# Optimization experiments

Hardware: AMD Instinct MI355X
Metric: run time of the kernel (lower is better)

The kernel has to match this reference:

```python
import jax, jax.numpy as jnp
import numpy as np
from jax.scipy.linalg import block_diag

NI, NO, NU, NH, NB = 32, 2, 10, 1024, 16384   # num_input, num_output, num_u, num_hidden, batch
N = NU // NO                                   # MPC horizon N = 5
M_INEQ = NU + NI * (N - 1)                     # 138 inequality constraints
EPS = 1e-4                                     # Q = L L^T + eps I
BN_EPS = 1e-5                                  # torch BatchNorm1d default eps
IPM_ITERS = 30                                 # fixed primal-dual interior-point iterations
NEG_SLOPE = 0.2
SIGMA = 0.1                                    # centering parameter


def setup_inputs():
    key = jax.random.key(0)
    k = jax.random.split(key, 12)
    u = lambda kk, shape, lim: jax.random.uniform(kk, shape, jnp.float32, -lim, lim)
    return {
        "x": jax.random.normal(k[0], (NB, NI), jnp.float32),
        "fc1_w": u(k[1], (NH, NI), 1.0 / np.sqrt(NI)),
        "fc1_b": u(k[2], (NH,), 1.0 / np.sqrt(NI)),
        "fc2_w": u(k[3], (NU, NH), 1.0 / np.sqrt(NH)),
        "fc2_b": u(k[4], (NU,), 1.0 / np.sqrt(NH)),
        "bn1_g": jnp.ones((NH,), jnp.float32),
        "bn1_b": jnp.zeros((NH,), jnp.float32),
        "bn2_g": jnp.ones((NU,), jnp.float32),
        "bn2_b": jnp.zeros((NU,), jnp.float32),
        "L": jnp.tril(jax.random.uniform(k[5], (NI, NI), dtype=jnp.float32)),
        "L_P": jnp.tril(jax.random.uniform(k[6], (NI, NI), dtype=jnp.float32)),
        "L_R": jnp.tril(jax.random.uniform(k[7], (NO, NO), dtype=jnp.float32)),
        "A": u(k[8], (NI, NI), 1.0) * 0.1,   # scaled for stable A^k powers in B_hat
        "Bm": u(k[9], (NI, NO), 1.0),
        "u0": jnp.zeros((NU,), jnp.float32),
        "s0": jnp.ones((M_INEQ,), jnp.float32),
    }


def _bn(x, g, b):
    # training-mode BatchNorm1d: biased batch statistics
    mu = jnp.mean(x, axis=0)
    var = jnp.mean(jnp.square(x - mu), axis=0)
    return (x - mu) * jax.lax.rsqrt(var + BN_EPS) * g + b


def _build_qp(L, L_P, L_R, A, Bm, u0, s0):
    # Q = (tril mask * L)(...)^T + eps I, same for P (state) and R (input) costs
    Lm = jnp.tril(L);   Q = Lm @ Lm.T + EPS * jnp.eye(NI, dtype=L.dtype)
    Lp = jnp.tril(L_P); P = Lp @ Lp.T + EPS * jnp.eye(NI, dtype=L.dtype)
    Lr = jnp.tril(L_R); R = Lr @ Lr.T + EPS * jnp.eye(NO, dtype=L.dtype)
    # B_hat: lower block-Toeplitz with block (i,j) = A^{i-j} B for j<=i  -> [NI*(N-1), NU]
    pows = [Bm]
    for _ in range(N - 2):
        pows.append(A @ pows[-1])
    zero = jnp.zeros((NI, NO), dtype=L.dtype)
    rows = []
    for i in range(N - 1):
        blocks = [pows[i - j] for j in range(i + 1)] + [zero] * (N - 1 - i)
        rows.append(jnp.concatenate(blocks, axis=1))
    B_hat = jnp.concatenate(rows, axis=0)
    Q_diag = block_diag(*([Q] * (N - 2) + [P]))        # diag(Q,...,Q,P)
    R_diag = block_diag(*([R] * N))                    # diag(R,...,R)
    Q_hat = B_hat.T @ Q_diag @ B_hat + R_diag          # [NU, NU]
    G = jnp.concatenate([jnp.eye(NU, dtype=L.dtype), B_hat], axis=0)  # [M_INEQ, NU]
    h = G @ u0 + s0
    return Q_hat, G, h


def _ipm_qp(Qm, p, G, h):
    """Batched primal-dual interior point: min_z 1/2 z^T Qm z + p^T z  s.t.  G z <= h.
    Qm [nz,nz], G [m,nz], h [m] shared; p [B,nz] batched. Returns z* [B,nz]."""
    B, nz = p.shape
    m = G.shape[0]

    def step(carry, _):
        z, s, lam = carry
        rd = z @ Qm + p + lam @ G                 # dual residual (Qm symmetric)
        rp = z @ G.T + s - h                      # primal residual
        mu = jnp.mean(s * lam, axis=-1, keepdims=True)
        rc = s * lam - SIGMA * mu                 # centered complementarity
        w = lam / s                               # [B, m]
        H = Qm + jnp.einsum('mi,bm,mj->bij', G, w, G)   # [B, nz, nz]
        rhs = -(rd + ((lam * rp - rc) / s) @ G)         # [B, nz]
        dz = jnp.linalg.solve(H, rhs[..., None])[..., 0]
        ds = -rp - dz @ G.T
        dlam = (-rc - lam * ds) / s
        # fraction-to-boundary step keeping s, lam > 0
        rs = jnp.where(ds < 0, -s / jnp.where(ds < 0, ds, -1.0), jnp.inf)
        rl = jnp.where(dlam < 0, -lam / jnp.where(dlam < 0, dlam, -1.0), jnp.inf)
        alpha = jnp.minimum(1.0, 0.99 * jnp.minimum(jnp.min(rs, -1), jnp.min(rl, -1)))[:, None]
        return (z + alpha * dz, s + alpha * ds, lam + alpha * dlam), None

    z0 = jnp.zeros_like(p)
    s_init = jnp.ones((B, m), p.dtype)
    l_init = jnp.ones((B, m), p.dtype)
    (z, _, _), _ = jax.lax.scan(step, (z0, s_init, l_init), None, length=IPM_ITERS)
    return z


def reference(x, fc1_w, fc1_b, fc2_w, fc2_b, bn1_g, bn1_b, bn2_g, bn2_b,
              L, L_P, L_R, A, Bm, u0, s0):
    h1 = jax.nn.leaky_relu(x @ fc1_w.T + fc1_b, NEG_SLOPE)
    h1 = _bn(h1, bn1_g, bn1_b)
    p = jax.nn.leaky_relu(h1 @ fc2_w.T + fc2_b, NEG_SLOPE)
    p = _bn(p, bn2_g, bn2_b)                       # [B, NU] = linear cost of QP
    Q_hat, G, hvec = _build_qp(L, L_P, L_R, A, Bm, u0, s0)
    z = _ipm_qp(Q_hat, p, G, hvec)                 # [B, NU]
    return z[:, 0]                                 # z @ e0 (weight = [1,0,...,0])


if __name__ == '__main__':
    out = reference(**setup_inputs())
    print(out.shape, out[:4])
```

## Files before the change

### kernel.cpp

```cpp
#include <hip/hip_runtime.h>
#include <math.h>

#define NIx 32
#define NOx 2
#define NUx 10
#define NHx 1024
#define NBx 16384
#define MIx 138
#define EPSQ 1e-4f
#define BNEPS 1e-5f
#define ITERS 30
#define SLOPE 0.2f
#define SIGMA_C 0.1f

#define QM_OFF 0
#define G_OFF 128
#define H_OFF 1856
#define P2_OFF 2048
#define P1S_OFF 2368
#define P1Q_OFF 6464
#define PRAW_OFF 10560

__device__ __forceinline__ float frcp(float x){ return __builtin_amdgcn_rcpf(x); }
__device__ __forceinline__ float frsq(float x){ return __builtin_amdgcn_rsqf(x); }
__device__ __forceinline__ float lrelu(float x){ return x > 0.0f ? x : SLOPE * x; }

typedef float v2f __attribute__((ext_vector_type(2)));
__device__ __forceinline__ v2f make2(float a, float b){ v2f r; r.x = a; r.y = b; return r; }
__device__ __forceinline__ v2f splat2(float a){ v2f r; r.x = a; r.y = a; return r; }
__device__ __forceinline__ v2f pkfma(v2f a, v2f b, v2f c){ return __builtin_elementwise_fma(a, b, c); }
__device__ __forceinline__ v2f pkmax(v2f a, v2f b){ return __builtin_elementwise_max(a, b); }

template<int CTRL>
__device__ __forceinline__ float dpp_mov(float x){
    int y = __builtin_amdgcn_update_dpp(0, __float_as_int(x), CTRL, 0xF, 0xF, true);
    return __int_as_float(y);
}
__device__ __forceinline__ float red8_add(float x){
    x += dpp_mov<0xB1>(x);
    x += dpp_mov<0x4E>(x);
    x += dpp_mov<0x141>(x);
    return x;
}
__device__ __forceinline__ float red8_max(float x){
    x = fmaxf(x, dpp_mov<0xB1>(x));
    x = fmaxf(x, dpp_mov<0x4E>(x));
    x = fmaxf(x, dpp_mov<0x141>(x));
    return x;
}

__global__ __launch_bounds__(256) void k_buildstats(const float* L, const float* LP, const float* LR,
                                                    const float* A, const float* Bm,
                                                    const float* u0, const float* s0,
                                                    const float* x, const float* w1, const float* b1,
                                                    float* ws){
    __shared__ float sL[1024], sLP[1024], sA[1024], sQ[1024], sP[1024];
    __shared__ float sPow[4][64];
    __shared__ float sBh[128*10];
    __shared__ float sQB[128*10];
    __shared__ float sR[3];
    __shared__ __align__(16) float sX[1024];
    int t = threadIdx.x;
    if (blockIdx.x < 2048){
        int rb = blockIdx.x >> 2;
        int cb = blockIdx.x & 3;
        int c = cb * 256 + t;
        const float4* wg4 = (const float4*)(w1 + (size_t)c * 32);
        float4 wr[8];
        #pragma unroll
        for (int q = 0; q < 8; ++q) wr[q] = wg4[q];
        float bc = b1[c];
        int r0 = rb * 32;
        const float4* xg4 = (const float4*)x + (size_t)r0 * 8;
        float4* sX4 = (float4*)sX;
        sX4[t] = xg4[t];
        __syncthreads();
        float sum = 0.0f, sq = 0.0f;
        #pragma unroll 2
        for (int r = 0; r < 32; ++r){
            const float4* xr4 = sX4 + r * 8;
            float a0 = 0, a1 = 0, a2 = 0, a3 = 0;
            #pragma unroll
            for (int q = 0; q < 8; ++q){
                float4 v = xr4[q];
                a0 = fmaf(v.x, wr[q].x, a0);
                a1 = fmaf(v.y, wr[q].y, a1);
                a2 = fmaf(v.z, wr[q].z, a2);
                a3 = fmaf(v.w, wr[q].w, a3);
            }
            float h = lrelu((a0 + a1) + (a2 + a3) + bc);
            sum += h; sq = fmaf(h, h, sq);
        }
        int buf = (rb & 3) * 1024 + c;
        atomicAdd(&ws[P1S_OFF + buf], sum);
        atomicAdd(&ws[P1Q_OFF + buf], sq);
        return;
    }
    for (int idx = t; idx < 1024; idx += 256){
        int i = idx >> 5, j = idx & 31;
        sL[idx]  = (j <= i) ? L[idx]  : 0.0f;
        sLP[idx] = (j <= i) ? LP[idx] : 0.0f;
        sA[idx]  = A[idx];
    }
    if (t < 64) sPow[0][t] = Bm[t];
    if (t == 0){
        float a = LR[0], b = LR[2], c = LR[3];
        sR[0] = a*a + EPSQ; sR[1] = a*b; sR[2] = b*b + c*c + EPSQ;
    }
    __syncthreads();
    for (int idx = t; idx < 1024; idx += 256){
        int i = idx >> 5, j = idx & 31;
        float q = 0.0f, p = 0.0f;
        for (int k = 0; k < 32; ++k){
            q = fmaf(sL[i*32+k],  sL[j*32+k],  q);
            p = fmaf(sLP[i*32+k], sLP[j*32+k], p);
        }
        if (i == j){ q += EPSQ; p += EPSQ; }
        sQ[idx] = q; sP[idx] = p;
    }
    for (int kp = 1; kp < 4; ++kp){
        __syncthreads();
        if (t < 64){
            int i = t >> 1, c = t & 1;
            float a = 0.0f;
            for (int j = 0; j < 32; ++j) a = fmaf(sA[i*32+j], sPow[kp-1][j*2+c], a);
            sPow[kp][t] = a;
        }
    }
    __syncthreads();
    for (int idx = t; idx < 1280; idx += 256){
        int r = idx / 10, c = idx % 10;
        int bi = r >> 5, ri = r & 31, bj = c >> 1, cj = c & 1;
        sBh[idx] = (bj <= bi) ? sPow[bi-bj][ri*2+cj] : 0.0f;
    }
    __syncthreads();
    for (int idx = t; idx < 1280; idx += 256){
        int r = idx / 10, c = idx % 10;
        int bi = r >> 5, ri = r & 31;
        const float* Qd = (bi < 3) ? sQ : sP;
        float a = 0.0f;
        for (int k = 0; k < 32; ++k) a = fmaf(Qd[ri*32+k], sBh[(bi*32+k)*10+c], a);
        sQB[idx] = a;
    }
    __syncthreads();
    if (t < 120){
        int i = t / 12, j = t % 12;
        float a = 0.0f;
        if (j < 10){
            for (int r = 0; r < 128; ++r) a = fmaf(sBh[r*10+i], sQB[r*10+j], a);
            if ((i >> 1) == (j >> 1)) a += sR[(i&1)+(j&1)];
        }
        ws[QM_OFF + t] = a;
    }
    for (int idx = t; idx < 144*12; idx += 256){
        int m = idx / 12, i = idx % 12;
        float v = 0.0f;
        if (i < 10 && m < MIx) v = (m < 10) ? ((i == m) ? 1.0f : 0.0f) : sBh[(m-10)*10 + i];
        ws[G_OFF + idx] = v;
    }
    for (int m = t; m < 144; m += 256){
        float hv = 0.0f;
        if (m < MIx){
            hv = s0[m];
            if (m < 10) hv += u0[m];
            else { for (int i = 0; i < 10; ++i) hv = fmaf(sBh[(m-10)*10+i], u0[i], hv); }
        }
        ws[H_OFF + m] = hv;
    }
}

__global__ __launch_bounds__(1024) void k_fc2(const float* __restrict__ x, const float* __restrict__ w1,
                                              const float* __restrict__ w2, const float* __restrict__ b1v,
                                              const float* __restrict__ b2v, const float* __restrict__ g1,
                                              const float* __restrict__ bb1, float* __restrict__ ws){
    __shared__ __align__(16) float sPool[10240];
    __shared__ float sA1[1024], sC1[1024];
    int t = threadIdx.x;
    if (t < 1024){
        int k = t;
        float ssum = 0.0f, qsum = 0.0f;
        #pragma unroll
        for (int b = 0; b < 4; ++b){
            ssum += ws[P1S_OFF + b*1024 + k];
            qsum += ws[P1Q_OFF + b*1024 + k];
        }
        float mu  = ssum * (1.0f/16384.0f);
        float var = qsum * (1.0f/16384.0f) - mu*mu;
        float a1 = g1[k] / sqrtf(var + BNEPS);
        sA1[k] = a1;
        sC1[k] = bb1[k] - mu * a1;
    }
    int r = t & 63;
    int q = t >> 6;
    int row = blockIdx.x * 64 + r;
    const float4* xg4 = (const float4*)(x + (size_t)row * 32);
    float4 xr[8];
    #pragma unroll
    for (int i = 0; i < 8; ++i) xr[i] = xg4[i];
    float acc[10];
    #pragma unroll
    for (int j = 0; j < 10; ++j) acc[j] = 0.0f;
    const float4* w1g4 = (const float4*)w1;
    float4* sW4 = (float4*)sPool;
    for (int ch = 0; ch < 8; ++ch){
        __syncthreads();
        if (t < 1024) sW4[t] = w1g4[ch*1024 + t];
        __syncthreads();
        #pragma unroll
        for (int i = 0; i < 8; ++i){
            int klc = __builtin_amdgcn_readfirstlane(q*8 + i);
            int kl  = __builtin_amdgcn_readfirstlane(ch*128 + klc);
            const float4* wv4 = sW4 + klc*8;
            float a0 = 0, a1 = 0, a2 = 0, a3 = 0;
            #pragma unroll
            for (int u = 0; u < 8; ++u){
                float4 wv = wv4[u];
                float4 xv = xr[u];
                a0 = fmaf(xv.x, wv.x, a0);
                a1 = fmaf(xv.y, wv.y, a1);
                a2 = fmaf(xv.z, wv.z, a2);
                a3 = fmaf(xv.w, wv.w, a3);
            }
            float h = fmaf(lrelu((a0 + a1) + (a2 + a3) + b1v[kl]), sA1[kl], sC1[kl]);
            #pragma unroll
            for (int j = 0; j < 10; ++j) acc[j] = fmaf(h, w2[j*1024 + kl], acc[j]);
        }
    }
    __syncthreads();
    float* pacc = sPool;
    #pragma unroll
    for (int j = 0; j < 10; ++j) pacc[t*10 + j] = acc[j];
    __syncthreads();
    if (t < 64){
        float pv[10];
        #pragma unroll
        for (int j = 0; j < 10; ++j){
            float a = b2v[j];
            #pragma unroll
            for (int w = 0; w < 16; ++w) a += pacc[(w*64 + t)*10 + j];
            pv[j] = lrelu(a);
        }
        #pragma unroll
        for (int j = 0; j < 10; ++j) ws[PRAW_OFF + (size_t)(blockIdx.x*64 + t)*10 + j] = pv[j];
        float sv[10], qv[10];
        #pragma unroll
        for (int j = 0; j < 10; ++j){ sv[j] = pv[j]; qv[j] = pv[j]*pv[j]; }
        #pragma unroll
        for (int m = 1; m < 64; m <<= 1){
            #pragma unroll
            for (int j = 0; j < 10; ++j){
                sv[j] += __shfl_xor(sv[j], m);
                qv[j] += __shfl_xor(qv[j], m);
            }
        }
        if (t == 0){
            int base = P2_OFF + (blockIdx.x & 15) * 20;
            #pragma unroll
            for (int j = 0; j < 10; ++j){
                atomicAdd(&ws[base + j], sv[j]);
                atomicAdd(&ws[base + 10 + j], qv[j]);
            }
        }
    }
}

#define TIX(i,j) ((i)*((i)+1)/2 + (j))

#define PSTEPA(P, B, GP) { \
    v2f sv = s2[P], lv = lam2[P]; \
    v2f isv; isv.x = frcp(sv.x); isv.y = frcp(sv.y); \
    v2f wv = lv * isv; \
    v2f r = sv - *(const v2f*)(sHH2 + (P)*16 + lg*2); \
    _Pragma("unroll") \
    for (int _i = 0; _i < (B); ++_i) r = pkfma(splat2(z[_i]), GP[_i], r); \
    rp2[P] = r; \
    sl2 = pkfma(sv, lv, sl2); \
    _Pragma("unroll") \
    for (int _i = 0; _i < (B); ++_i){ \
        v2f wg = wv * GP[_i]; \
        _Pragma("unroll") \
        for (int _j = 0; _j <= _i; ++_j) Hm2[TIX(_i,_j)] = pkfma(wg, GP[_j], Hm2[TIX(_i,_j)]); \
    } }

#define PSTEPB(P, B, GP) { \
    v2f sv = s2[P], lv = lam2[P]; \
    v2f isv; isv.x = frcp(sv.x); isv.y = frcp(sv.y); \
    v2f coef = pkfma(lv, rp2[P], smu2) * isv; \
    _Pragma("unroll") \
    for (int _i = 0; _i < (B); ++_i) racc2[_i] = pkfma(coef, GP[_i], racc2[_i]); }

#define PSTEPC(P, B, GP) { \
    v2f dotv = splat2(0.0f); \
    _Pragma("unroll") \
    for (int _i = 0; _i < (B); ++_i) dotv = pkfma(splat2(dz[_i]), GP[_i], dotv); \
    v2f sv = s2[P], lv = lam2[P]; \
    v2f isv; isv.x = frcp(sv.x); isv.y = frcp(sv.y); \
    v2f dsv = -(rp2[P] + dotv); \
    v2f rcv = pkfma(sv, lv, nsmu2); \
    v2f dlv = -(pkfma(lv, dsv, rcv) * isv); \
    ds2[P] = dsv; dl2[P] = dlv; \
    v2f ilv; ilv.x = frcp(lv.x); ilv.y = frcp(lv.y); \
    av2 = pkmax(av2, pkmax((-dsv)*isv, (-dlv)*ilv)); }

#define LOADP(GP, PP) v2f GP[8]; { \
    const float4* _g4 = (const float4*)(sG3 + lg*36 + (PP)*16); \
    float4 _a = _g4[0], _b = _g4[1], _c = _g4[2], _d = _g4[3]; \
    GP[0] = make2(_a.x,_a.y); GP[1] = make2(_a.z,_a.w); \
    GP[2] = make2(_b.x,_b.y); GP[3] = make2(_b.z,_b.w); \
    GP[4] = make2(_c.x,_c.y); GP[5] = make2(_c.z,_c.w); \
    GP[6] = make2(_d.x,_d.y); GP[7] = make2(_d.z,_d.w); }

__global__ __launch_bounds__(64, 2) void k_ipm(const float* __restrict__ ws, const float* __restrict__ g2v,
                                               const float* __restrict__ bb2, float* __restrict__ out){
    __shared__ __align__(16) float sQm[120];
    __shared__ __align__(16) float sQt2[72];
    __shared__ __align__(16) float sPV[8*12];
    __shared__ __align__(16) float sG3[8*36];
    __shared__ __align__(16) float sHH2[128];
    __shared__ float sA2[10], sC2[10];
    int t = threadIdx.x;
    for (int i = t; i < 120; i += 64) sQm[i] = ws[QM_OFF + i];
    if (t < 36){
        int i = 0;
        #pragma unroll
        for (int r = 1; r < 8; ++r) if (TIX(r,0) <= t) i = r;
        int j = t - TIX(i,0);
        sQt2[t*2]   = ws[QM_OFF + i*12 + j] * 0.125f;
        sQt2[t*2+1] = 0.0f;
    }
    if (t < 10){
        float ssum = 0.0f, qsum = 0.0f;
        #pragma unroll
        for (int b = 0; b < 16; ++b){
            ssum += ws[P2_OFF + b*20 + t];
            qsum += ws[P2_OFF + b*20 + 10 + t];
        }
        float mu  = ssum * (1.0f/16384.0f);
        float var = qsum * (1.0f/16384.0f) - mu*mu;
        float a2 = g2v[t] / sqrtf(var + BNEPS);
        sA2[t] = a2;
        sC2[t] = bb2[t] - mu * a2;
    }
    __syncthreads();

    int lg = t & 7;
    int eidx = t >> 3;
    int elem = blockIdx.x * 8 + eidx;
    const float* GB = ws + G_OFF;
    const float4* sQm4 = (const float4*)sQm;

    for (int i = t; i < 80; i += 64){
        int e = i / 10, c = i - e*10;
        int el = blockIdx.x * 8 + e;
        sPV[e*12 + c] = fmaf(ws[PRAW_OFF + (size_t)el*10 + c], sA2[c], sC2[c]);
    }
    for (int i = t; i < 128; i += 64){
        int c = i & 1, lgx = (i >> 1) & 7, p = i >> 4;
        int row = 10 + (p >> 1)*32 + (2*(p & 1) + c)*8 + lgx;
        sHH2[p*16 + lgx*2 + c] = ws[H_OFF + row];
    }
    for (int i = t; i < 256; i += 64){
        int c = i & 1, ii = (i >> 1) & 7, pp = (i >> 4) & 1, lgx = i >> 5;
        int row = 106 + (pp*2 + c)*8 + lgx;
        sG3[lgx*36 + pp*16 + ii*2 + c] = GB[row*12 + ii];
    }
    v2f g0[2], g1[2], g2r[4], g3r[4], g4r[6], g5r[6];
    {
        int ra, rb;
        ra = 10 + lg; rb = 18 + lg;
        #pragma unroll
        for (int i = 0; i < 2; ++i) g0[i] = make2(GB[ra*12+i], GB[rb*12+i]);
        ra = 26 + lg; rb = 34 + lg;
        #pragma unroll
        for (int i = 0; i < 2; ++i) g1[i] = make2(GB[ra*12+i], GB[rb*12+i]);
        ra = 42 + lg; rb = 50 + lg;
        #pragma unroll
        for (int i = 0; i < 4; ++i) g2r[i] = make2(GB[ra*12+i], GB[rb*12+i]);
        ra = 58 + lg; rb = 66 + lg;
        #pragma unroll
        for (int i = 0; i < 4; ++i) g3r[i] = make2(GB[ra*12+i], GB[rb*12+i]);
        ra = 74 + lg; rb = 82 + lg;
        #pragma unroll
        for (int i = 0; i < 6; ++i) g4r[i] = make2(GB[ra*12+i], GB[rb*12+i]);
        ra = 90 + lg; rb = 98 + lg;
        #pragma unroll
        for (int i = 0; i < 6; ++i) g5r[i] = make2(GB[ra*12+i], GB[rb*12+i]);
    }
    float h16 = ws[H_OFF + lg];
    float h17 = (lg < 2) ? ws[H_OFF + 8 + lg] : 1.0f;
    __syncthreads();

    float z[10];
    #pragma unroll
    for (int i = 0; i < 10; ++i) z[i] = 0.0f;
    v2f s2[8], lam2[8];
    #pragma unroll
    for (int p = 0; p < 8; ++p){ s2[p] = splat2(1.0f); lam2[p] = splat2(1.0f); }
    float s16v = 1.0f, s17v = 1.0f, lam16v = 1.0f;
    float lam17v = (lg < 2) ? 1.0f : 0.0f;

    #pragma unroll 1
    for (int it = 0; it < ITERS; ++it){
        v2f Hm2[36];
        {
            const v2f* qt2 = (const v2f*)sQt2;
            #pragma unroll
            for (int i = 0; i < 36; ++i) Hm2[i] = qt2[i];
        }
        v2f sl2 = splat2(0.0f);
        v2f rp2[8];
        float rp16, rp17;
        PSTEPA(0, 2, g0)  PSTEPA(1, 2, g1)
        PSTEPA(2, 4, g2r) PSTEPA(3, 4, g3r)
        PSTEPA(4, 6, g4r) PSTEPA(5, 6, g5r)
        { LOADP(gv, 0) PSTEPA(6, 8, gv) }
        { LOADP(gv, 1) PSTEPA(7, 8, gv) }
        float w16, w17, sl_s;
        {
            float zs = z[0];
            #pragma unroll
            for (int i = 1; i < 8; ++i) zs = (lg == i) ? z[i] : zs;
            rp16 = zs + s16v - h16;
            sl_s = s16v * lam16v;
            w16 = lam16v * frcp(s16v);
            float zs17 = (lg == 1) ? z[9] : z[8];
            rp17 = zs17 + s17v - h17;
            sl_s = fmaf(s17v, lam17v, sl_s);
            w17 = lam17v * frcp(s17v);
        }
        float Hm[55];
        #pragma unroll
        for (int i = 0; i < 36; ++i) Hm[i] = Hm2[i].x + Hm2[i].y;
        #pragma unroll
        for (int i = 0; i < 8; ++i) Hm[TIX(i,i)] += (lg == i) ? w16 : 0.0f;
        float d88 = (lg == 0) ? w17 : 0.0f;
        float d99 = (lg == 1) ? w17 : 0.0f;
        float sl = sl2.x + sl2.y + sl_s;
        #pragma unroll
        for (int i = 0; i < 36; ++i) Hm[i] = red8_add(Hm[i]);
        d88 = red8_add(d88);
        d99 = red8_add(d99);
        sl = red8_add(sl);
        float smu = SIGMA_C * sl * (1.0f/138.0f);
        __asm__ __volatile__("" ::: "memory");
        v2f smu2 = splat2(smu);
        v2f racc2[8];
        #pragma unroll
        for (int i = 0; i < 8; ++i) racc2[i] = splat2(0.0f);
        PSTEPB(0, 2, g0)  PSTEPB(1, 2, g1)
        PSTEPB(2, 4, g2r) PSTEPB(3, 4, g3r)
        PSTEPB(4, 6, g4r) PSTEPB(5, 6, g5r)
        { LOADP(gv, 0) PSTEPB(6, 8, gv) }
        { LOADP(gv, 1) PSTEPB(7, 8, gv) }
        float coef16 = frcp(s16v) * fmaf(lam16v, rp16, smu);
        float coef17 = frcp(s17v) * fmaf(lam17v, rp17, smu);
        coef17 = (lg < 2) ? coef17 : 0.0f;
        float rs[10];
        #pragma unroll
        for (int i = 0; i < 8; ++i){
            float v = racc2[i].x + racc2[i].y;
            v += (lg == i) ? coef16 : 0.0f;
            rs[i] = red8_add(v);
        }
        rs[8] = red8_add((lg == 0) ? coef17 : 0.0f);
        rs[9] = red8_add((lg == 1) ? coef17 : 0.0f);
        v2f rhs2[5];
        {
            const float4* pv4 = (const float4*)(sPV + eidx*12);
            float4 pa = pv4[0], pb = pv4[1];
            const float2* pv2 = (const float2*)(sPV + eidx*12 + 8);
            float2 pc = pv2[0];
            rhs2[0] = make2(-(pa.x + rs[0]), -(pa.y + rs[1]));
            rhs2[1] = make2(-(pa.z + rs[2]), -(pa.w + rs[3]));
            rhs2[2] = make2(-(pb.x + rs[4]), -(pb.y + rs[5]));
            rhs2[3] = make2(-(pb.z + rs[6]), -(pb.w + rs[7]));
            rhs2[4] = make2(-(pc.x + rs[8]), -(pc.y + rs[9]));
        }
        #pragma unroll
        for (int j = 0; j < 10; ++j){
            float4 qa = sQm4[j*3+0], qb = sQm4[j*3+1], qc = sQm4[j*3+2];
            v2f mz = splat2(-z[j]);
            rhs2[0] = pkfma(mz, make2(qa.x, qa.y), rhs2[0]);
            rhs2[1] = pkfma(mz, make2(qa.z, qa.w), rhs2[1]);
            rhs2[2] = pkfma(mz, make2(qb.x, qb.y), rhs2[2]);
            rhs2[3] = pkfma(mz, make2(qb.z, qb.w), rhs2[3]);
            rhs2[4] = pkfma(mz, make2(qc.x, qc.y), rhs2[4]);
            if (j >= 8){
                float q[10] = {qa.x,qa.y,qa.z,qa.w, qb.x,qb.y,qb.z,qb.w, qc.x,qc.y};
                #pragma unroll
                for (int i = 0; i <= j; ++i) Hm[TIX(j,i)] = q[i];
            }
        }
        Hm[TIX(8,8)] += d88;
        Hm[TIX(9,9)] += d99;
        float rhs[10] = {rhs2[0].x, rhs2[0].y, rhs2[1].x, rhs2[1].y, rhs2[2].x,
                         rhs2[2].y, rhs2[3].x, rhs2[3].y, rhs2[4].x, rhs2[4].y};
        #pragma unroll
        for (int j = 0; j < 10; ++j){
            float d = Hm[TIX(j,j)];
            #pragma unroll
            for (int k2 = 0; k2 < j; ++k2){ float v = Hm[TIX(j,k2)]; d = fmaf(-v, v, d); }
            d = fmaxf(d, 1e-30f);
            float rinv = frsq(d);
            Hm[TIX(j,j)] = rinv;
            #pragma unroll
            for (int i = j+1; i < 10; ++i){
                float v2 = Hm[TIX(i,j)];
                #pragma unroll
                for (int k2 = 0; k2 < j; ++k2) v2 = fmaf(-Hm[TIX(i,k2)], Hm[TIX(j,k2)], v2);
                Hm[TIX(i,j)] = v2 * rinv;
            }
        }
        #pragma unroll
        for (int i = 0; i < 10; ++i){
            float v2 = rhs[i];
            #pragma unroll
            for (int k2 = 0; k2 < i; ++k2) v2 = fmaf(-Hm[TIX(i,k2)], rhs[k2], v2);
            rhs[i] = v2 * Hm[TIX(i,i)];
        }
        float dz[10];
        #pragma unroll
        for (int i = 9; i >= 0; --i){
            float v2 = rhs[i];
            #pragma unroll
            for (int k2 = i+1; k2 < 10; ++k2) v2 = fmaf(-Hm[TIX(k2,i)], dz[k2], v2);
            dz[i] = v2 * Hm[TIX(i,i)];
        }
        __asm__ __volatile__("" ::: "memory");
        v2f nsmu2 = splat2(-smu);
        v2f ds2[8], dl2[8];
        v2f av2 = splat2(0.0f);
        PSTEPC(0, 2, g0)  PSTEPC(1, 2, g1)
        PSTEPC(2, 4, g2r) PSTEPC(3, 4, g3r)
        PSTEPC(4, 6, g4r) PSTEPC(5, 6, g5r)
        { LOADP(gv, 0) PSTEPC(6, 8, gv) }
        { LOADP(gv, 1) PSTEPC(7, 8, gv) }
        float ds16, dl16, ds17, dl17;
        float ainv = fmaxf(av2.x, av2.y);
        {
            float dzs = dz[0];
            #pragma unroll
            for (int i = 1; i < 8; ++i) dzs = (lg == i) ? dz[i] : dzs;
            float dsk = -rp16 - dzs;
            float isk = frcp(s16v);
            float rc = fmaf(s16v, lam16v, -smu);
            float dlk = -(rc + lam16v * dsk) * isk;
            ds16 = dsk; dl16 = dlk;
            ainv = fmaxf(ainv, fmaxf(-dsk * isk, -dlk * frcp(lam16v)));
        }
        {
            float dzs = (lg == 1) ? dz[9] : dz[8];
            bool val = lg < 2;
            float dsk = val ? (-rp17 - dzs) : 0.0f;
            float isk = frcp(s17v);
            float rc = fmaf(s17v, lam17v, -smu);
            float dlk = -(rc + lam17v * dsk) * isk;
            dlk = val ? dlk : 0.0f;
            ds17 = dsk; dl17 = dlk;
            float cand = fmaxf(-dsk * isk, -dlk * frcp(lam17v));
            ainv = fmaxf(ainv, val ? cand : 0.0f);
        }
        ainv = red8_max(ainv);
        float alpha = fminf(1.0f, 0.99f * frcp(fmaxf(ainv, 1e-30f)));
        v2f al2 = splat2(alpha);
        #pragma unroll
        for (int i = 0; i < 10; ++i) z[i] = fmaf(alpha, dz[i], z[i]);
        #pragma unroll
        for (int p = 0; p < 8; ++p){
            s2[p]   = pkfma(al2, ds2[p], s2[p]);
            lam2[p] = pkfma(al2, dl2[p], lam2[p]);
        }
        s16v   = fmaf(alpha, ds16, s16v);
        s17v   = fmaf(alpha, ds17, s17v);
        lam16v = fmaf(alpha, dl16, lam16v);
        lam17v = fmaf(alpha, dl17, lam17v);
    }
    if (lg == 0) out[elem] = z[0];
}

extern "C" void kernel_launch(void* const* d_in, const int* in_sizes, int n_in,
                              void* d_out, int out_size, void* d_ws, size_t ws_size,
                              hipStream_t stream){
    const float* x   = (const float*)d_in[0];
    const float* w1  = (const float*)d_in[1];
    const float* b1  = (const float*)d_in[2];
    const float* w2  = (const float*)d_in[3];
    const float* b2  = (const float*)d_in[4];
    const float* g1  = (const float*)d_in[5];
    const float* bb1 = (const float*)d_in[6];
    const float* g2  = (const float*)d_in[7];
    const float* bb2 = (const float*)d_in[8];
    const float* L   = (const float*)d_in[9];
    const float* LP  = (const float*)d_in[10];
    const float* LR  = (const float*)d_in[11];
    const float* A   = (const float*)d_in[12];
    const float* Bm  = (const float*)d_in[13];
    const float* u0  = (const float*)d_in[14];
    const float* s0  = (const float*)d_in[15];
    float* ws  = (float*)d_ws;
    float* out = (float*)d_out;

    hipMemsetAsync(ws + P2_OFF, 0, (P1Q_OFF + 4096 - P2_OFF) * sizeof(float), stream);
    hipLaunchKernelGGL(k_buildstats, dim3(2049), dim3(256), 0, stream,
                       L, LP, LR, A, Bm, u0, s0, x, w1, b1, ws);
    hipLaunchKernelGGL(k_fc2, dim3(256), dim3(1024), 0, stream, x, w1, w2, b1, b2, g1, bb1, ws);
    hipLaunchKernelGGL(k_ipm, dim3(2048), dim3(64), 0, stream, ws, g2, bb2, out);
}
```

Measured before the change: 307.7 us.

## Repartition fc2 into smaller blocks and pre-transpose w2 for paired loads

The fused fc1/fc2 kernel changes from 256 blocks of 1024 threads to 2048 blocks of 256 threads. Each block now handles 8 rows and splits the hidden dimension across lanes, combining partial sums with cross-lane shuffles before a small shared-memory reduction. An extra block in the stats kernel transposes w2 into the workspace so each hidden unit's weight pairs can be read as float2. The stats kernel's shared memory is also aliased into one pool and the QB intermediate moves to global memory, to allow more blocks per CU. The aim is better occupancy, at the cost of every block recomputing the BN1 affine terms and re-streaming all of w1, plus more atomic contention on the fc2 statistics.

```diff
diff --git a/kernel.cpp b/kernel.cpp
--- a/kernel.cpp
+++ b/kernel.cpp
@@ -20,6 +20,7 @@
 #define P1S_OFF 2368
 #define P1Q_OFF 6464
 #define PRAW_OFF 10560
+#define W2T_OFF 174400
 
 __device__ __forceinline__ float frcp(float x){ return __builtin_amdgcn_rcpf(x); }
 __device__ __forceinline__ float frsq(float x){ return __builtin_amdgcn_rsqf(x); }
@@ -49,17 +50,12 @@
     return x;
 }
 
-__global__ __launch_bounds__(256) void k_buildstats(const float* L, const float* LP, const float* LR,
-                                                    const float* A, const float* Bm,
-                                                    const float* u0, const float* s0,
-                                                    const float* x, const float* w1, const float* b1,
-                                                    float* ws){
-    __shared__ float sL[1024], sLP[1024], sA[1024], sQ[1024], sP[1024];
-    __shared__ float sPow[4][64];
-    __shared__ float sBh[128*10];
-    __shared__ float sQB[128*10];
-    __shared__ float sR[3];
-    __shared__ __align__(16) float sX[1024];
+__global__ __launch_bounds__(256, 8) void k_buildstats(const float* L, const float* LP, const float* LR,
+                                                       const float* A, const float* Bm,
+                                                       const float* u0, const float* s0,
+                                                       const float* x, const float* w1, const float* b1,
+                                                       const float* w2, float* ws){
+    __shared__ __align__(16) float pool[5120];
     int t = threadIdx.x;
     if (blockIdx.x < 2048){
         int rb = blockIdx.x >> 2;
@@ -72,7 +68,7 @@
         float bc = b1[c];
         int r0 = rb * 32;
         const float4* xg4 = (const float4*)x + (size_t)r0 * 8;
-        float4* sX4 = (float4*)sX;
+        float4* sX4 = (float4*)pool;
         sX4[t] = xg4[t];
         __syncthreads();
         float sum = 0.0f, sq = 0.0f;
@@ -96,16 +92,30 @@
         atomicAdd(&ws[P1Q_OFF + buf], sq);
         return;
     }
+    if (blockIdx.x == 2049){
+        for (int idx = t; idx < 10240; idx += 256){
+            int p = idx / 2048;
+            int rem = idx - p*2048;
+            int kl = rem >> 1, c = rem & 1;
+            ws[W2T_OFF + idx] = w2[(size_t)(2*p + c)*1024 + kl];
+        }
+        return;
+    }
+    float* sL  = pool;
+    float* sLP = pool + 1024;
+    float* sA  = pool + 2048;
+    float* sQ  = pool + 3072;
+    float* sP  = pool + 4096;
+    float* sBh = pool;
+    float* sPow= pool + 1536;
+    float* sR  = pool + 1792;
+    float* gQB = ws + PRAW_OFF;
+
     for (int idx = t; idx < 1024; idx += 256){
         int i = idx >> 5, j = idx & 31;
         sL[idx]  = (j <= i) ? L[idx]  : 0.0f;
         sLP[idx] = (j <= i) ? LP[idx] : 0.0f;
         sA[idx]  = A[idx];
-    }
-    if (t < 64) sPow[0][t] = Bm[t];
-    if (t == 0){
-        float a = LR[0], b = LR[2], c = LR[3];
-        sR[0] = a*a + EPSQ; sR[1] = a*b; sR[2] = b*b + c*c + EPSQ;
     }
     __syncthreads();
     for (int idx = t; idx < 1024; idx += 256){
@@ -118,20 +128,26 @@
         if (i == j){ q += EPSQ; p += EPSQ; }
         sQ[idx] = q; sP[idx] = p;
     }
+    __syncthreads();
+    if (t < 64) sPow[t] = Bm[t];
+    if (t == 0){
+        float a = LR[0], b = LR[2], c = LR[3];
+        sR[0] = a*a + EPSQ; sR[1] = a*b; sR[2] = b*b + c*c + EPSQ;
+    }
     for (int kp = 1; kp < 4; ++kp){
         __syncthreads();
         if (t < 64){
             int i = t >> 1, c = t & 1;
             float a = 0.0f;
-            for (int j = 0; j < 32; ++j) a = fmaf(sA[i*32+j], sPow[kp-1][j*2+c], a);
-            sPow[kp][t] = a;
+            for (int j = 0; j < 32; ++j) a = fmaf(sA[i*32+j], sPow[(kp-1)*64 + j*2+c], a);
+            sPow[kp*64 + t] = a;
         }
     }
     __syncthreads();
     for (int idx = t; idx < 1280; idx += 256){
         int r = idx / 10, c = idx % 10;
         int bi = r >> 5, ri = r & 31, bj = c >> 1, cj = c & 1;
-        sBh[idx] = (bj <= bi) ? sPow[bi-bj][ri*2+cj] : 0.0f;
+        sBh[idx] = (bj <= bi) ? sPow[(bi-bj)*64 + ri*2+cj] : 0.0f;
     }
     __syncthreads();
     for (int idx = t; idx < 1280; idx += 256){
@@ -140,14 +156,14 @@
         const float* Qd = (bi < 3) ? sQ : sP;
         float a = 0.0f;
         for (int k = 0; k < 32; ++k) a = fmaf(Qd[ri*32+k], sBh[(bi*32+k)*10+c], a);
-        sQB[idx] = a;
+        gQB[idx] = a;
     }
     __syncthreads();
     if (t < 120){
         int i = t / 12, j = t % 12;
         float a = 0.0f;
         if (j < 10){
-            for (int r = 0; r < 128; ++r) a = fmaf(sBh[r*10+i], sQB[r*10+j], a);
+            for (int r = 0; r < 128; ++r) a = fmaf(sBh[r*10+i], gQB[r*10+j], a);
             if ((i >> 1) == (j >> 1)) a += sR[(i&1)+(j&1)];
         }
         ws[QM_OFF + t] = a;
@@ -169,15 +185,15 @@
     }
 }
 
-__global__ __launch_bounds__(1024) void k_fc2(const float* __restrict__ x, const float* __restrict__ w1,
-                                              const float* __restrict__ w2, const float* __restrict__ b1v,
-                                              const float* __restrict__ b2v, const float* __restrict__ g1,
-                                              const float* __restrict__ bb1, float* __restrict__ ws){
-    __shared__ __align__(16) float sPool[10240];
+__global__ __launch_bounds__(256, 7) void k_fc2(const float* __restrict__ x, const float* __restrict__ w1,
+                                                const float* __restrict__ b1v, const float* __restrict__ b2v,
+                                                const float* __restrict__ g1, const float* __restrict__ bb1,
+                                                float* __restrict__ ws){
+    __shared__ __align__(16) float sW[64*36];
     __shared__ float sA1[1024], sC1[1024];
+    __shared__ float pacc[320];
     int t = threadIdx.x;
-    if (t < 1024){
-        int k = t;
+    for (int k = t; k < 1024; k += 256){
         float ssum = 0.0f, qsum = 0.0f;
         #pragma unroll
         for (int b = 0; b < 4; ++b){
@@ -190,9 +206,9 @@
         sA1[k] = a1;
         sC1[k] = bb1[k] - mu * a1;
     }
-    int r = t & 63;
-    int q = t >> 6;
-    int row = blockIdx.x * 64 + r;
+    int r = t & 7;
+    int sl = t >> 3;
+    int row = blockIdx.x * 8 + r;
     const float4* xg4 = (const float4*)(x + (size_t)row * 32);
     float4 xr[8];
     #pragma unroll
@@ -200,17 +216,20 @@
     float acc[10];
     #pragma unroll
     for (int j = 0; j < 10; ++j) acc[j] = 0.0f;
-    const float4* w1g4 = (const float4*)w1;
-    float4* sW4 = (float4*)sPool;
-    for (int ch = 0; ch < 8; ++ch){
+    const float* w2t = ws + W2T_OFF;
+    for (int ch = 0; ch < 16; ++ch){
         __syncthreads();
-        if (t < 1024) sW4[t] = w1g4[ch*1024 + t];
+        #pragma unroll
+        for (int idx = t; idx < 512; idx += 256){
+            int rr = idx >> 3, cc = idx & 7;
+            ((float4*)(sW + rr*36))[cc] = ((const float4*)(w1 + (size_t)(ch*64 + rr)*32))[cc];
+        }
         __syncthreads();
         #pragma unroll
-        for (int i = 0; i < 8; ++i){
-            int klc = __builtin_amdgcn_readfirstlane(q*8 + i);
-            int kl  = __builtin_amdgcn_readfirstlane(ch*128 + klc);
-            const float4* wv4 = sW4 + klc*8;
+        for (int i = 0; i < 2; ++i){
+            int klc = sl*2 + i;
+            int kl = ch*64 + klc;
+            const float4* wv4 = (const float4*)(sW + klc*36);
             float a0 = 0, a1 = 0, a2 = 0, a3 = 0;
             #pragma unroll
             for (int u = 0; u < 8; ++u){
@@ -223,30 +242,41 @@
             }
             float h = fmaf(lrelu((a0 + a1) + (a2 + a3) + b1v[kl]), sA1[kl], sC1[kl]);
             #pragma unroll
-            for (int j = 0; j < 10; ++j) acc[j] = fmaf(h, w2[j*1024 + kl], acc[j]);
-        }
-    }
-    __syncthreads();
-    float* pacc = sPool;
+            for (int p = 0; p < 5; ++p){
+                float2 w2p = *(const float2*)(w2t + p*2048 + kl*2);
+                acc[2*p]   = fmaf(h, w2p.x, acc[2*p]);
+                acc[2*p+1] = fmaf(h, w2p.y, acc[2*p+1]);
+            }
+        }
+    }
     #pragma unroll
-    for (int j = 0; j < 10; ++j) pacc[t*10 + j] = acc[j];
-    __syncthreads();
-    if (t < 64){
+    for (int m = 8; m < 64; m <<= 1){
+        #pragma unroll
+        for (int j = 0; j < 10; ++j) acc[j] += __shfl_xor(acc[j], m);
+    }
+    __syncthreads();
+    if ((t & 63) < 8){
+        int w = t >> 6;
+        #pragma unroll
+        for (int j = 0; j < 10; ++j) pacc[(w*8 + r)*10 + j] = acc[j];
+    }
+    __syncthreads();
+    if (t < 8){
         float pv[10];
         #pragma unroll
         for (int j = 0; j < 10; ++j){
             float a = b2v[j];
             #pragma unroll
-            for (int w = 0; w < 16; ++w) a += pacc[(w*64 + t)*10 + j];
+            for (int w = 0; w < 4; ++w) a += pacc[(w*8 + t)*10 + j];
             pv[j] = lrelu(a);
         }
         #pragma unroll
-        for (int j = 0; j < 10; ++j) ws[PRAW_OFF + (size_t)(blockIdx.x*64 + t)*10 + j] = pv[j];
+        for (int j = 0; j < 10; ++j) ws[PRAW_OFF + (size_t)(blockIdx.x*8 + t)*10 + j] = pv[j];
         float sv[10], qv[10];
         #pragma unroll
         for (int j = 0; j < 10; ++j){ sv[j] = pv[j]; qv[j] = pv[j]*pv[j]; }
         #pragma unroll
-        for (int m = 1; m < 64; m <<= 1){
+        for (int m = 1; m < 8; m <<= 1){
             #pragma unroll
             for (int j = 0; j < 10; ++j){
                 sv[j] += __shfl_xor(sv[j], m);
@@ -601,8 +631,8 @@
     float* out = (float*)d_out;
 
     hipMemsetAsync(ws + P2_OFF, 0, (P1Q_OFF + 4096 - P2_OFF) * sizeof(float), stream);
-    hipLaunchKernelGGL(k_buildstats, dim3(2049), dim3(256), 0, stream,
-                       L, LP, LR, A, Bm, u0, s0, x, w1, b1, ws);
-    hipLaunchKernelGGL(k_fc2, dim3(256), dim3(1024), 0, stream, x, w1, w2, b1, b2, g1, bb1, ws);
+    hipLaunchKernelGGL(k_buildstats, dim3(2050), dim3(256), 0, stream,
+                       L, LP, LR, A, Bm, u0, s0, x, w1, b1, w2, ws);
+    hipLaunchKernelGGL(k_fc2, dim3(2048), dim3(256), 0, stream, x, w1, b1, b2, g1, bb1, ws);
     hipLaunchKernelGGL(k_ipm, dim3(2048), dim3(64), 0, stream, ws, g2, bb2, out);
 }
```

Result: slower. 653.5 us (+112.4%).
